# Performance work log

Hardware: AMD Instinct MI355X
Metric: run time of the kernel (lower is better)

The kernel has to match this reference:

```python
import jax, jax.numpy as jnp
import numpy as np

N, K, H, T = 65536, 8, 128, 4  # nodes, max children, h_size, n_types


def setup_inputs() -> dict:
    key = jax.random.key(0)
    ks = jax.random.split(key, 8)
    h = jax.random.normal(ks[0], (N, K, H), jnp.float32)          # mailbox child hidden states
    c = jax.random.normal(ks[1], (N, K, H), jnp.float32)          # mailbox child cell states
    f_input = jax.random.normal(ks[2], (N, H), jnp.float32)       # precomputed x @ W_f per node
    type_id = jax.random.randint(ks[3], (N,), 0, T, jnp.int32)    # node type for dispatch
    scale = 0.05
    U_iou = jax.random.normal(ks[4], (T, H, 3 * H), jnp.float32) * scale  # per-type i,o,u recurrent mats
    b_iou = jax.random.normal(ks[5], (T, 3 * H), jnp.float32) * scale
    U_f = jax.random.normal(ks[6], (T, H, H), jnp.float32) * scale        # per-type forget-gate mat
    b_f = jax.random.normal(ks[7], (T, H), jnp.float32) * scale
    return dict(h=h, c=c, f_input=f_input, type_id=type_id,
                U_iou=U_iou, b_iou=b_iou, U_f=U_f, b_f=b_f)


def reference(h, c, f_input, type_id, U_iou, b_iou, U_f, b_f):
    """TypedTreeCell.reduce_func: per-type TreeLSTM child aggregation.

    Returns concat([iou_aggr, c_aggr], -1) of shape [N, 4*H].
    """
    n_types = U_iou.shape[0]
    n_nodes = h.shape[0]
    h_size = h.shape[2]
    h_sum = h.sum(axis=1)  # [N, H] child-sum for i,o,u gates
    iou_aggr = jnp.zeros((n_nodes, 3 * h_size), h.dtype)
    c_aggr = jnp.zeros((n_nodes, h_size), h.dtype)
    for t in range(n_types):  # fixed small type loop mirrors the module's dispatch
        m = (type_id == t)[:, None]
        iou_t = h_sum @ U_iou[t] + b_iou[t]                                  # [N, 3H]
        f_t = jax.nn.sigmoid(f_input[:, None, :] + h @ U_f[t] + b_f[t])     # [N, K, H]
        c_t = (f_t * c).sum(axis=1)                                          # [N, H]
        iou_aggr = jnp.where(m, iou_t, iou_aggr)
        c_aggr = jnp.where(m, c_t, c_aggr)
    return jnp.concatenate([iou_aggr, c_aggr], axis=-1)
```

## Files before the change

kernel.cpp:

```cpp
#include <hip/hip_runtime.h>
#include <cstdint>


typedef __bf16 bf16;
typedef bf16 bf16x8 __attribute__((ext_vector_type(8)));
typedef float f32x4 __attribute__((ext_vector_type(4)));

#define N_NODES 65536
#define KCH 8
#define HSZ 128
#define T_TYPES 4
#define TM 16
#define LDS_STRIDE 136

#define WS_PERM_OFF   256
#define WS_PREUF_OFF  (WS_PERM_OFF + 4*N_NODES)
#define WS_PREUIOU_OFF (WS_PREUF_OFF + 131072)

__global__ void k_count(const int* __restrict__ ta, int* __restrict__ ws_i) {
    int i = blockIdx.x * blockDim.x + threadIdx.x;
    int t = ta[i];
    int lane = threadIdx.x & 63;
    #pragma unroll
    for (int tt = 0; tt < T_TYPES; ++tt) {
        unsigned long long m = __ballot(t == tt);
        int leader = __ffsll((unsigned long long)m) - 1;
        if (t == tt && lane == leader)
            atomicAdd(&ws_i[tt], (int)__popcll(m));
    }
}

__global__ void k_offsets(int* ws_i) {
    if (threadIdx.x == 0 && blockIdx.x == 0) {
        int acc = 0;
        for (int t = 0; t < T_TYPES; ++t) {
            ws_i[8 + t] = acc;
            ws_i[4 + t] = acc;
            acc += ws_i[t];
        }
    }
}

__global__ void k_scatter(const int* __restrict__ ta, int* __restrict__ ws_i,
                          int* __restrict__ perm) {
    int i = blockIdx.x * blockDim.x + threadIdx.x;
    int t = ta[i];
    int lane = threadIdx.x & 63;
    #pragma unroll
    for (int tt = 0; tt < T_TYPES; ++tt) {
        unsigned long long m = __ballot(t == tt);
        if (t == tt) {
            int leader = __ffsll((unsigned long long)m) - 1;
            int base = 0;
            if (lane == leader) base = atomicAdd(&ws_i[4 + tt], (int)__popcll(m));
            base = __shfl(base, leader, 64);
            int rank = (int)__popcll(m & ((1ull << lane) - 1ull));
            perm[base + rank] = i;
        }
    }
}

__global__ void k_swz_uf(const float* __restrict__ U, bf16* __restrict__ dst) {
    int idx = blockIdx.x * blockDim.x + threadIdx.x;
    int t = idx >> 14;
    int r = (idx >> 7) & 127;
    int j = idx & 127;
    float v = U[idx];
    int kblk = r >> 5, kin = r & 31;
    int lane = ((kin >> 3) << 4) | (j & 15);
    int e = kin & 7;
    int cb = j >> 4;
    dst[((((t * 4 + kblk) * 8 + cb) * 64 + lane) << 3) + e] = (bf16)v;
}

__global__ void k_swz_uiou(const float* __restrict__ U, bf16* __restrict__ dst) {
    int idx = blockIdx.x * blockDim.x + threadIdx.x;
    int t = idx / 49152;
    int rm = idx - t * 49152;
    int r = rm / 384;
    int j = rm - r * 384;
    float v = U[idx];
    int kblk = r >> 5, kin = r & 31;
    int lane = ((kin >> 3) << 4) | (j & 15);
    int e = kin & 7;
    int cb = j >> 4;
    dst[((((t * 4 + kblk) * 24 + cb) * 64 + lane) << 3) + e] = (bf16)v;
}

__global__ __launch_bounds__(256, 2) void k_main(
    const float* __restrict__ h, const float* __restrict__ c,
    const float* __restrict__ f_input,
    const float* __restrict__ b_iou, const float* __restrict__ b_f,
    const int* __restrict__ perm, const int* __restrict__ ws_i,
    const bf16* __restrict__ preUf, const bf16* __restrict__ preUiou,
    float* __restrict__ out)
{
    const int t = blockIdx.y;
    const int tile = blockIdx.x;
    const int cnt = ws_i[t];
    if (tile * TM >= cnt) return;
    const int base = ws_i[8 + t] + tile * TM;
    const int rem = min(TM, cnt - tile * TM);

    __shared__ __align__(16) bf16 hs[(128 + 16) * LDS_STRIDE];
    bf16* hsum = hs + 128 * LDS_STRIDE;

    const int tid = threadIdx.x;
    const int w = tid >> 6;
    const int l = tid & 63;
    const int lu = l & 15;
    const int g = l >> 4;

    {
        int mloc = w * 4 + g;
        int mc = mloc < rem ? mloc : 0;
        long gn = perm[base + mc];
        const float* hp = h + gn * (long)(KCH * HSZ) + lu * 8;
        float sarr[8];
        #pragma unroll
        for (int i = 0; i < 8; ++i) sarr[i] = 0.f;
        #pragma unroll
        for (int k = 0; k < KCH; ++k) {
            const float4* p = (const float4*)(hp + k * HSZ);
            float4 a = p[0], b = p[1];
            sarr[0] += a.x; sarr[1] += a.y; sarr[2] += a.z; sarr[3] += a.w;
            sarr[4] += b.x; sarr[5] += b.y; sarr[6] += b.z; sarr[7] += b.w;
            bf16x8 v;
            v[0] = (bf16)a.x; v[1] = (bf16)a.y; v[2] = (bf16)a.z; v[3] = (bf16)a.w;
            v[4] = (bf16)b.x; v[5] = (bf16)b.y; v[6] = (bf16)b.z; v[7] = (bf16)b.w;
            *((bf16x8*)&hs[(mloc * KCH + k) * LDS_STRIDE + lu * 8]) = v;
        }
        bf16x8 sv;
        #pragma unroll
        for (int i = 0; i < 8; ++i) sv[i] = (bf16)sarr[i];
        *((bf16x8*)&hsum[mloc * LDS_STRIDE + lu * 8]) = sv;
    }
    __syncthreads();

    f32x4 acc[8][2];
    #pragma unroll
    for (int rt = 0; rt < 8; ++rt)
        #pragma unroll
        for (int cb = 0; cb < 2; ++cb)
            acc[rt][cb] = (f32x4){0.f, 0.f, 0.f, 0.f};

    const bf16x8* Bf = (const bf16x8*)preUf;
    #pragma unroll
    for (int kb = 0; kb < 4; ++kb) {
        bf16x8 b0 = Bf[((t * 4 + kb) * 8 + w * 2 + 0) * 64 + l];
        bf16x8 b1 = Bf[((t * 4 + kb) * 8 + w * 2 + 1) * 64 + l];
        #pragma unroll
        for (int rt = 0; rt < 8; ++rt) {
            bf16x8 a = *((const bf16x8*)&hs[(rt * 16 + lu) * LDS_STRIDE + kb * 32 + g * 8]);
            acc[rt][0] = __builtin_amdgcn_mfma_f32_16x16x32_bf16(a, b0, acc[rt][0], 0, 0, 0);
            acc[rt][1] = __builtin_amdgcn_mfma_f32_16x16x32_bf16(a, b1, acc[rt][1], 0, 0, 0);
        }
    }

    {
        const int col0 = w * 32 + lu;
        const float bf0 = b_f[t * HSZ + col0];
        const float bf1 = b_f[t * HSZ + col0 + 16];
        #pragma unroll
        for (int rt = 0; rt < 8; ++rt) {
            int m = rt * 2 + (g >> 1);
            int mc = m < rem ? m : 0;
            long gn = perm[base + mc];
            #pragma unroll
            for (int cb = 0; cb < 2; ++cb) {
                int col = col0 + cb * 16;
                float fiv = f_input[gn * HSZ + col];
                float bfv = cb ? bf1 : bf0;
                float p = 0.f;
                #pragma unroll
                for (int r = 0; r < 4; ++r) {
                    int k = ((g & 1) << 2) + r;
                    float s = acc[rt][cb][r] + fiv + bfv;
                    float fg = 1.0f / (1.0f + __expf(-s));
                    float cv = c[(gn * KCH + k) * HSZ + col];
                    p += fg * cv;
                }
                p += __shfl_xor(p, 16, 64);
                if (((g & 1) == 0) && m < rem)
                    out[gn * (4 * HSZ) + 3 * HSZ + col] = p;
            }
        }
    }

    f32x4 acc2[6];
    #pragma unroll
    for (int cf = 0; cf < 6; ++cf) acc2[cf] = (f32x4){0.f, 0.f, 0.f, 0.f};
    const bf16x8* Bi = (const bf16x8*)preUiou;
    #pragma unroll
    for (int kb = 0; kb < 4; ++kb) {
        bf16x8 a = *((const bf16x8*)&hsum[lu * LDS_STRIDE + kb * 32 + g * 8]);
        #pragma unroll
        for (int cf = 0; cf < 6; ++cf) {
            bf16x8 b = Bi[((t * 4 + kb) * 24 + w * 6 + cf) * 64 + l];
            acc2[cf] = __builtin_amdgcn_mfma_f32_16x16x32_bf16(a, b, acc2[cf], 0, 0, 0);
        }
    }
    {
        long gns[4]; bool ok[4];
        #pragma unroll
        for (int r = 0; r < 4; ++r) {
            int m = g * 4 + r;
            ok[r] = m < rem;
            gns[r] = perm[base + (ok[r] ? m : 0)];
        }
        #pragma unroll
        for (int cf = 0; cf < 6; ++cf) {
            int col = w * 96 + cf * 16 + lu;
            float bi = b_iou[t * 384 + col];
            #pragma unroll
            for (int r = 0; r < 4; ++r)
                if (ok[r]) out[gns[r] * (4 * HSZ) + col] = acc2[cf][r] + bi;
        }
    }
}

extern "C" void kernel_launch(void* const* d_in, const int* in_sizes, int n_in,
                              void* d_out, int out_size, void* d_ws, size_t ws_size,
                              hipStream_t stream) {
    const float* h       = (const float*)d_in[0];
    const float* c       = (const float*)d_in[1];
    const float* f_input = (const float*)d_in[2];
    const int*   type_id = (const int*)d_in[3];
    const float* U_iou   = (const float*)d_in[4];
    const float* b_iou   = (const float*)d_in[5];
    const float* U_f     = (const float*)d_in[6];
    const float* b_f     = (const float*)d_in[7];
    float* out = (float*)d_out;

    char* ws = (char*)d_ws;
    int* ws_i = (int*)ws;
    int* perm = (int*)(ws + WS_PERM_OFF);
    bf16* preUf = (bf16*)(ws + WS_PREUF_OFF);
    bf16* preUiou = (bf16*)(ws + WS_PREUIOU_OFF);

    hipMemsetAsync(ws, 0, 64, stream);
    k_swz_uf  <<<(T_TYPES * HSZ * HSZ) / 256, 256, 0, stream>>>(U_f, preUf);
    k_swz_uiou<<<(T_TYPES * HSZ * 3 * HSZ) / 256, 256, 0, stream>>>(U_iou, preUiou);
    k_count   <<<N_NODES / 256, 256, 0, stream>>>(type_id, ws_i);
    k_offsets <<<1, 64, 0, stream>>>(ws_i);
    k_scatter <<<N_NODES / 256, 256, 0, stream>>>(type_id, ws_i, perm);

    dim3 grid(N_NODES / TM, T_TYPES);
    k_main<<<grid, 256, 0, stream>>>(h, c, f_input, b_iou, b_f,
                                     perm, ws_i, preUf, preUiou, out);
}
```

Measured before the change: 738.1 us.

## Compact tile grid, widen blocks to 512 threads, stage forget-gate via LDS

```diff
diff --git a/kernel.cpp b/kernel.cpp
--- a/kernel.cpp
+++ b/kernel.cpp
@@ -4,6 +4,7 @@
 
 typedef __bf16 bf16;
 typedef bf16 bf16x8 __attribute__((ext_vector_type(8)));
+typedef bf16 bf16x4 __attribute__((ext_vector_type(4)));
 typedef float f32x4 __attribute__((ext_vector_type(4)));
 
 #define N_NODES 65536
@@ -32,12 +33,16 @@
 
 __global__ void k_offsets(int* ws_i) {
     if (threadIdx.x == 0 && blockIdx.x == 0) {
-        int acc = 0;
+        int acc = 0, tacc = 0;
         for (int t = 0; t < T_TYPES; ++t) {
+            int cnt = ws_i[t];
             ws_i[8 + t] = acc;
             ws_i[4 + t] = acc;
-            acc += ws_i[t];
-        }
+            ws_i[12 + t] = tacc;
+            acc += cnt;
+            tacc += (cnt + TM - 1) / TM;
+        }
+        ws_i[16] = tacc;
     }
 }
 
@@ -60,34 +65,35 @@
     }
 }
 
-__global__ void k_swz_uf(const float* __restrict__ U, bf16* __restrict__ dst) {
+__global__ void k_swz(const float* __restrict__ Uf, const float* __restrict__ Uiou,
+                      bf16* __restrict__ dstf, bf16* __restrict__ dstiou) {
     int idx = blockIdx.x * blockDim.x + threadIdx.x;
-    int t = idx >> 14;
-    int r = (idx >> 7) & 127;
-    int j = idx & 127;
-    float v = U[idx];
-    int kblk = r >> 5, kin = r & 31;
-    int lane = ((kin >> 3) << 4) | (j & 15);
-    int e = kin & 7;
-    int cb = j >> 4;
-    dst[((((t * 4 + kblk) * 8 + cb) * 64 + lane) << 3) + e] = (bf16)v;
-}
-
-__global__ void k_swz_uiou(const float* __restrict__ U, bf16* __restrict__ dst) {
-    int idx = blockIdx.x * blockDim.x + threadIdx.x;
-    int t = idx / 49152;
-    int rm = idx - t * 49152;
-    int r = rm / 384;
-    int j = rm - r * 384;
-    float v = U[idx];
-    int kblk = r >> 5, kin = r & 31;
-    int lane = ((kin >> 3) << 4) | (j & 15);
-    int e = kin & 7;
-    int cb = j >> 4;
-    dst[((((t * 4 + kblk) * 24 + cb) * 64 + lane) << 3) + e] = (bf16)v;
-}
-
-__global__ __launch_bounds__(256, 2) void k_main(
+    if (idx < T_TYPES * HSZ * HSZ) {
+        int t = idx >> 14;
+        int r = (idx >> 7) & 127;
+        int j = idx & 127;
+        float v = Uf[idx];
+        int kblk = r >> 5, kin = r & 31;
+        int lane = ((kin >> 3) << 4) | (j & 15);
+        int e = kin & 7;
+        int cb = j >> 4;
+        dstf[((((t * 4 + kblk) * 8 + cb) * 64 + lane) << 3) + e] = (bf16)v;
+    } else {
+        int i2 = idx - T_TYPES * HSZ * HSZ;
+        int t = i2 / 49152;
+        int rm = i2 - t * 49152;
+        int r = rm / 384;
+        int j = rm - r * 384;
+        float v = Uiou[i2];
+        int kblk = r >> 5, kin = r & 31;
+        int lane = ((kin >> 3) << 4) | (j & 15);
+        int e = kin & 7;
+        int cb = j >> 4;
+        dstiou[((((t * 4 + kblk) * 24 + cb) * 64 + lane) << 3) + e] = (bf16)v;
+    }
+}
+
+__global__ __launch_bounds__(512, 4) void k_main(
     const float* __restrict__ h, const float* __restrict__ c,
     const float* __restrict__ f_input,
     const float* __restrict__ b_iou, const float* __restrict__ b_f,
@@ -95,10 +101,15 @@
     const bf16* __restrict__ preUf, const bf16* __restrict__ preUiou,
     float* __restrict__ out)
 {
-    const int t = blockIdx.y;
-    const int tile = blockIdx.x;
+    const int b = blockIdx.x;
+    if (b >= ws_i[16]) return;
+    int t;
+    if (b < ws_i[13]) t = 0;
+    else if (b < ws_i[14]) t = 1;
+    else if (b < ws_i[15]) t = 2;
+    else t = 3;
+    const int tile = b - ws_i[12 + t];
     const int cnt = ws_i[t];
-    if (tile * TM >= cnt) return;
     const int base = ws_i[8 + t] + tile * TM;
     const int rem = min(TM, cnt - tile * TM);
 
@@ -106,98 +117,76 @@
     bf16* hsum = hs + 128 * LDS_STRIDE;
 
     const int tid = threadIdx.x;
-    const int w = tid >> 6;
+    const int w2 = tid >> 6;
     const int l = tid & 63;
     const int lu = l & 15;
     const int g = l >> 4;
 
     {
-        int mloc = w * 4 + g;
-        int mc = mloc < rem ? mloc : 0;
+        int node = w2 * 2 + (g >> 1);
+        int khalf = (g & 1) * 4;
+        int mc = node < rem ? node : 0;
         long gn = perm[base + mc];
         const float* hp = h + gn * (long)(KCH * HSZ) + lu * 8;
         float sarr[8];
         #pragma unroll
         for (int i = 0; i < 8; ++i) sarr[i] = 0.f;
         #pragma unroll
-        for (int k = 0; k < KCH; ++k) {
+        for (int k0 = 0; k0 < 4; ++k0) {
+            int k = khalf + k0;
             const float4* p = (const float4*)(hp + k * HSZ);
-            float4 a = p[0], b = p[1];
+            float4 a = p[0], bb = p[1];
             sarr[0] += a.x; sarr[1] += a.y; sarr[2] += a.z; sarr[3] += a.w;
-            sarr[4] += b.x; sarr[5] += b.y; sarr[6] += b.z; sarr[7] += b.w;
+            sarr[4] += bb.x; sarr[5] += bb.y; sarr[6] += bb.z; sarr[7] += bb.w;
             bf16x8 v;
             v[0] = (bf16)a.x; v[1] = (bf16)a.y; v[2] = (bf16)a.z; v[3] = (bf16)a.w;
-            v[4] = (bf16)b.x; v[5] = (bf16)b.y; v[6] = (bf16)b.z; v[7] = (bf16)b.w;
-            *((bf16x8*)&hs[(mloc * KCH + k) * LDS_STRIDE + lu * 8]) = v;
-        }
-        bf16x8 sv;
-        #pragma unroll
-        for (int i = 0; i < 8; ++i) sv[i] = (bf16)sarr[i];
-        *((bf16x8*)&hsum[mloc * LDS_STRIDE + lu * 8]) = sv;
+            v[4] = (bf16)bb.x; v[5] = (bf16)bb.y; v[6] = (bf16)bb.z; v[7] = (bf16)bb.w;
+            *((bf16x8*)&hs[(node * KCH + k) * LDS_STRIDE + lu * 8]) = v;
+        }
+        #pragma unroll
+        for (int i = 0; i < 8; ++i) sarr[i] += __shfl_xor(sarr[i], 16, 64);
+        if ((g & 1) == 0) {
+            bf16x8 sv;
+            #pragma unroll
+            for (int i = 0; i < 8; ++i) sv[i] = (bf16)sarr[i];
+            *((bf16x8*)&hsum[node * LDS_STRIDE + lu * 8]) = sv;
+        }
     }
     __syncthreads();
 
-    f32x4 acc[8][2];
-    #pragma unroll
-    for (int rt = 0; rt < 8; ++rt)
+    f32x4 acc[4][2];
+    #pragma unroll
+    for (int rt = 0; rt < 4; ++rt)
         #pragma unroll
         for (int cb = 0; cb < 2; ++cb)
             acc[rt][cb] = (f32x4){0.f, 0.f, 0.f, 0.f};
 
+    const int rbase = (w2 >> 2) * 4;
+    const int cpair = (w2 & 3);
     const bf16x8* Bf = (const bf16x8*)preUf;
     #pragma unroll
     for (int kb = 0; kb < 4; ++kb) {
-        bf16x8 b0 = Bf[((t * 4 + kb) * 8 + w * 2 + 0) * 64 + l];
-        bf16x8 b1 = Bf[((t * 4 + kb) * 8 + w * 2 + 1) * 64 + l];
-        #pragma unroll
-        for (int rt = 0; rt < 8; ++rt) {
-            bf16x8 a = *((const bf16x8*)&hs[(rt * 16 + lu) * LDS_STRIDE + kb * 32 + g * 8]);
+        bf16x8 b0 = Bf[((t * 4 + kb) * 8 + cpair * 2 + 0) * 64 + l];
+        bf16x8 b1 = Bf[((t * 4 + kb) * 8 + cpair * 2 + 1) * 64 + l];
+        #pragma unroll
+        for (int rt = 0; rt < 4; ++rt) {
+            bf16x8 a = *((const bf16x8*)&hs[((rbase + rt) * 16 + lu) * LDS_STRIDE + kb * 32 + g * 8]);
             acc[rt][0] = __builtin_amdgcn_mfma_f32_16x16x32_bf16(a, b0, acc[rt][0], 0, 0, 0);
             acc[rt][1] = __builtin_amdgcn_mfma_f32_16x16x32_bf16(a, b1, acc[rt][1], 0, 0, 0);
         }
     }
 
-    {
-        const int col0 = w * 32 + lu;
-        const float bf0 = b_f[t * HSZ + col0];
-        const float bf1 = b_f[t * HSZ + col0 + 16];
-        #pragma unroll
-        for (int rt = 0; rt < 8; ++rt) {
-            int m = rt * 2 + (g >> 1);
-            int mc = m < rem ? m : 0;
-            long gn = perm[base + mc];
-            #pragma unroll
-            for (int cb = 0; cb < 2; ++cb) {
-                int col = col0 + cb * 16;
-                float fiv = f_input[gn * HSZ + col];
-                float bfv = cb ? bf1 : bf0;
-                float p = 0.f;
-                #pragma unroll
-                for (int r = 0; r < 4; ++r) {
-                    int k = ((g & 1) << 2) + r;
-                    float s = acc[rt][cb][r] + fiv + bfv;
-                    float fg = 1.0f / (1.0f + __expf(-s));
-                    float cv = c[(gn * KCH + k) * HSZ + col];
-                    p += fg * cv;
-                }
-                p += __shfl_xor(p, 16, 64);
-                if (((g & 1) == 0) && m < rem)
-                    out[gn * (4 * HSZ) + 3 * HSZ + col] = p;
-            }
-        }
-    }
-
-    f32x4 acc2[6];
-    #pragma unroll
-    for (int cf = 0; cf < 6; ++cf) acc2[cf] = (f32x4){0.f, 0.f, 0.f, 0.f};
+    f32x4 acc2[3];
+    #pragma unroll
+    for (int cf = 0; cf < 3; ++cf) acc2[cf] = (f32x4){0.f, 0.f, 0.f, 0.f};
     const bf16x8* Bi = (const bf16x8*)preUiou;
     #pragma unroll
     for (int kb = 0; kb < 4; ++kb) {
         bf16x8 a = *((const bf16x8*)&hsum[lu * LDS_STRIDE + kb * 32 + g * 8]);
         #pragma unroll
-        for (int cf = 0; cf < 6; ++cf) {
-            bf16x8 b = Bi[((t * 4 + kb) * 24 + w * 6 + cf) * 64 + l];
-            acc2[cf] = __builtin_amdgcn_mfma_f32_16x16x32_bf16(a, b, acc2[cf], 0, 0, 0);
+        for (int cf = 0; cf < 3; ++cf) {
+            bf16x8 bfr = Bi[((t * 4 + kb) * 24 + w2 * 3 + cf) * 64 + l];
+            acc2[cf] = __builtin_amdgcn_mfma_f32_16x16x32_bf16(a, bfr, acc2[cf], 0, 0, 0);
         }
     }
     {
@@ -209,13 +198,57 @@
             gns[r] = perm[base + (ok[r] ? m : 0)];
         }
         #pragma unroll
-        for (int cf = 0; cf < 6; ++cf) {
-            int col = w * 96 + cf * 16 + lu;
+        for (int cf = 0; cf < 3; ++cf) {
+            int col = (w2 * 3 + cf) * 16 + lu;
             float bi = b_iou[t * 384 + col];
             #pragma unroll
             for (int r = 0; r < 4; ++r)
                 if (ok[r]) out[gns[r] * (4 * HSZ) + col] = acc2[cf][r] + bi;
         }
+    }
+
+    __syncthreads();
+    {
+        const int col0 = cpair * 32 + lu;
+        const float bf0 = b_f[t * HSZ + col0];
+        const float bf1 = b_f[t * HSZ + col0 + 16];
+        #pragma unroll
+        for (int rt = 0; rt < 4; ++rt) {
+            #pragma unroll
+            for (int cb = 0; cb < 2; ++cb) {
+                #pragma unroll
+                for (int r = 0; r < 4; ++r) {
+                    int rc = (rbase + rt) * 16 + g * 4 + r;
+                    float s = acc[rt][cb][r] + (cb ? bf1 : bf0);
+                    hs[rc * LDS_STRIDE + col0 + cb * 16] = (bf16)s;
+                }
+            }
+        }
+    }
+    __syncthreads();
+
+    {
+        int m = tid >> 5;
+        int cg = tid & 31;
+        bool ok = m < rem;
+        long gn = perm[base + (ok ? m : 0)];
+        const float* crow = c + gn * (long)(KCH * HSZ) + cg * 4;
+        float4 fi = *(const float4*)(f_input + gn * HSZ + cg * 4);
+        float4 accv = {0.f, 0.f, 0.f, 0.f};
+        #pragma unroll
+        for (int k = 0; k < KCH; ++k) {
+            bf16x4 sv = *(const bf16x4*)&hs[(m * KCH + k) * LDS_STRIDE + cg * 4];
+            float4 cv = *(const float4*)(crow + k * HSZ);
+            float s0 = (float)sv[0] + fi.x;
+            float s1 = (float)sv[1] + fi.y;
+            float s2 = (float)sv[2] + fi.z;
+            float s3 = (float)sv[3] + fi.w;
+            accv.x += cv.x / (1.f + __expf(-s0));
+            accv.y += cv.y / (1.f + __expf(-s1));
+            accv.z += cv.z / (1.f + __expf(-s2));
+            accv.w += cv.w / (1.f + __expf(-s3));
+        }
+        if (ok) *((float4*)(out + gn * (4 * HSZ) + 3 * HSZ + cg * 4)) = accv;
     }
 }
 
@@ -238,14 +271,12 @@
     bf16* preUf = (bf16*)(ws + WS_PREUF_OFF);
     bf16* preUiou = (bf16*)(ws + WS_PREUIOU_OFF);
 
-    hipMemsetAsync(ws, 0, 64, stream);
-    k_swz_uf  <<<(T_TYPES * HSZ * HSZ) / 256, 256, 0, stream>>>(U_f, preUf);
-    k_swz_uiou<<<(T_TYPES * HSZ * 3 * HSZ) / 256, 256, 0, stream>>>(U_iou, preUiou);
-    k_count   <<<N_NODES / 256, 256, 0, stream>>>(type_id, ws_i);
-    k_offsets <<<1, 64, 0, stream>>>(ws_i);
-    k_scatter <<<N_NODES / 256, 256, 0, stream>>>(type_id, ws_i, perm);
-
-    dim3 grid(N_NODES / TM, T_TYPES);
-    k_main<<<grid, 256, 0, stream>>>(h, c, f_input, b_iou, b_f,
-                                     perm, ws_i, preUf, preUiou, out);
-}
+    hipMemsetAsync(ws, 0, 128, stream);
+    k_swz    <<<(T_TYPES * HSZ * HSZ + T_TYPES * HSZ * 3 * HSZ) / 256, 256, 0, stream>>>(U_f, U_iou, preUf, preUiou);
+    k_count  <<<N_NODES / 256, 256, 0, stream>>>(type_id, ws_i);
+    k_offsets<<<1, 64, 0, stream>>>(ws_i);
+    k_scatter<<<N_NODES / 256, 256, 0, stream>>>(type_id, ws_i, perm);
+
+    k_main<<<N_NODES / TM + T_TYPES, 512, 0, stream>>>(h, c, f_input, b_iou, b_f,
+                                                       perm, ws_i, preUf, preUiou, out);
+}
```

Result: faster. 708.8 us (-4.0%).
